# Optimization experiments

Hardware: AMD Instinct MI355X
Metric: run time of the kernel (lower is better)

## Reference

```python
import jax, jax.numpy as jnp
import numpy as np

BLOCK, HALO, HEADS = 8, 3, 4


def setup_inputs() -> dict:
    key = jax.random.key(0)
    k1, k2, k3, k4 = jax.random.split(key, 4)
    ch, d = 128, 128 // HEADS
    win = BLOCK + 2 * HALO
    return {
        "x": jax.random.normal(k1, (8, ch, 128, 128), dtype=jnp.float32),
        "qkv_w": jax.random.normal(k2, (3 * ch, ch), dtype=jnp.float32) * (2.0 / ch) ** 0.5,
        "rel_h": jax.random.normal(k3, (1, win, 1, d // 2), dtype=jnp.float32),
        "rel_w": jax.random.normal(k4, (1, 1, win, d // 2), dtype=jnp.float32),
    }


def _halo_windows(t, block, halo):
    b, c, h, w = t.shape
    win = block + 2 * halo
    nh, nw = h // block, w // block
    tp = jnp.pad(t, ((0, 0), (0, 0), (halo, halo), (halo, halo)))
    idx_h = (jnp.arange(nh) * block)[:, None] + jnp.arange(win)[None, :]
    idx_w = (jnp.arange(nw) * block)[:, None] + jnp.arange(win)[None, :]
    return tp[:, :, idx_h[:, None, :, None], idx_w[None, :, None, :]]


def reference(x, qkv_w, rel_h, rel_w):
    block, halo, heads = BLOCK, HALO, HEADS
    b, c, h, w = x.shape
    d = c // heads
    win = block + 2 * halo
    nh, nw = h // block, w // block

    # 1x1 conv (bias=False)
    qkv = jnp.einsum('bchw,oc->bohw', x, qkv_w)
    q, k, v = jnp.split(qkv, 3, axis=1)

    # q: non-overlapping blocks -> (b, nh, nw, heads, block*block, d), scaled
    q = q.reshape(b, heads, d, nh, block, nw, block)
    q = q.transpose(0, 3, 5, 1, 4, 6, 2).reshape(b, nh, nw, heads, block * block, d)
    q = q * d ** -0.5

    kw = _halo_windows(k, block, halo)
    vw = _halo_windows(v, block, halo)
    kw = kw.reshape(b, heads, d, nh, nw, win, win).transpose(0, 3, 4, 1, 5, 6, 2)
    vw = vw.reshape(b, heads, d, nh, nw, win, win).transpose(0, 3, 4, 1, 5, 6, 2)
    vw = vw.reshape(b, nh, nw, heads, win * win, d)

    # relative position bias added to keys (first half varies over rows, second over cols)
    k_h, k_w2 = jnp.split(kw, 2, axis=-1)
    kw = jnp.concatenate([k_h + rel_h, k_w2 + rel_w], axis=-1)
    kw = kw.reshape(b, nh, nw, heads, win * win, d)

    sim = jnp.einsum('...id,...jd->...ij', q, kw)
    attn = jax.nn.softmax(sim, axis=-1)
    out = jnp.einsum('...ij,...jd->...id', attn, vw)  # (b,nh,nw,heads, blk^2, d)

    # reassemble: channel = (head, d) head-major; rows = (nh, k1); cols = (nw, k2)
    out = out.reshape(b, nh, nw, heads, block, block, d)
    out = out.transpose(0, 3, 6, 1, 4, 2, 5).reshape(b, c, h, w)
    return out
```

## Files before the change

### kernel.cpp

```cpp
#include <hip/hip_runtime.h>
#include <hip/hip_bf16.h>


typedef __attribute__((ext_vector_type(8))) short bf16x8;
typedef __attribute__((ext_vector_type(4))) short bf16x4;
typedef __attribute__((ext_vector_type(4))) float f32x4;
union BF8 { bf16x8 v; unsigned u[4]; };
union BF4 { bf16x4 v; unsigned u[2]; };

#define DEVI static __device__ __forceinline__

DEVI short f2bf(float f) {
    __bf16 h = (__bf16)f;
    union { __bf16 h; short s; } c; c.h = h; return c.s;
}
DEVI unsigned pk2(float a, float b) {
    return (unsigned)(unsigned short)f2bf(a) | ((unsigned)(unsigned short)f2bf(b) << 16);
}

#if defined(__has_builtin)
#  if __has_builtin(__builtin_amdgcn_exp2f)
#    define EXP2(x) __builtin_amdgcn_exp2f(x)
#  else
#    define EXP2(x) exp2f(x)
#  endif
#else
#  define EXP2(x) exp2f(x)
#endif

#if defined(__has_builtin)
#  if __has_builtin(__builtin_amdgcn_mfma_f32_16x16x16bf16_1k)
#    define HAVE_MFMA16_1K 1
#  endif
#endif

DEVI f32x4 mfma16(bf16x4 a, bf16x4 b, f32x4 c) {
#ifdef HAVE_MFMA16_1K
    return __builtin_amdgcn_mfma_f32_16x16x16bf16_1k(a, b, c, 0, 0, 0);
#else
    f32x4 d;
    asm("v_mfma_f32_16x16x16_bf16 %0, %1, %2, %3" : "=v"(d) : "v"(a), "v"(b), "v"(c));
    return d;
#endif
}

#define QSCALE (0.17677669529663687f * 1.4426950408889634f)

__global__ void wcvt(const float* __restrict__ w, short* __restrict__ ws_w) {
    int e = blockIdx.x * 256 + threadIdx.x;
    if (e < 384 * 128) {
        float v = w[e];
        if (e < 128 * 128) v *= QSCALE;
        ws_w[e] = f2bf(v);
    }
}

__launch_bounds__(256)
__global__ void qkv_gemm(const float* __restrict__ x, const short* __restrict__ ws_w,
                         short* __restrict__ ws_q, short* __restrict__ ws_k,
                         short* __restrict__ ws_v) {
    const int blk = blockIdx.x;
    const int b = blk >> 6;
    const int pixbase = (blk & 63) << 8;
    const int tid = threadIdx.x, wv = tid >> 6, ln = tid & 63;
    const int lr = ln & 15, lg = ln >> 4;
    const int n0 = pixbase + wv * 64;
    const f32x4 zz = {0.f, 0.f, 0.f, 0.f};

    BF8 Bx[4][4];
    #pragma unroll
    for (int nt = 0; nt < 4; ++nt) {
        const int pix = n0 + nt * 16 + lr;
        #pragma unroll
        for (int ks = 0; ks < 4; ++ks) {
            const float* xp = x + (((size_t)((b << 7) + ks * 32 + lg * 8)) << 14) + pix;
            float f[8];
            #pragma unroll
            for (int e = 0; e < 8; ++e) f[e] = xp[(size_t)e << 14];
            Bx[nt][ks].u[0] = pk2(f[0], f[1]); Bx[nt][ks].u[1] = pk2(f[2], f[3]);
            Bx[nt][ks].u[2] = pk2(f[4], f[5]); Bx[nt][ks].u[3] = pk2(f[6], f[7]);
        }
    }

    for (int ot = 0; ot < 24; ++ot) {
        bf16x8 Aw[4];
        #pragma unroll
        for (int ks = 0; ks < 4; ++ks)
            Aw[ks] = *(const bf16x8*)&ws_w[(ot * 16 + lr) * 128 + ks * 32 + lg * 8];
        f32x4 acc[4];
        #pragma unroll
        for (int nt = 0; nt < 4; ++nt) {
            acc[nt] = zz;
            #pragma unroll
            for (int ks = 0; ks < 4; ++ks)
                acc[nt] = __builtin_amdgcn_mfma_f32_16x16x32_bf16(Aw[ks], Bx[nt][ks].v, acc[nt], 0, 0, 0);
        }
        if (ot < 8) {
            const int head = ot >> 1, dd0 = ((ot & 1) << 4) + lg * 4;
            #pragma unroll
            for (int nt = 0; nt < 4; ++nt) {
                const int pix = n0 + nt * 16 + lr;
                const int gr = pix >> 7, gc = pix & 127;
                const int ii = gr >> 3, jj = gc >> 3;
                const int qrow = ((gr & 7) << 3) | (gc & 7);
                size_t off = ((size_t)((((b * 16 + ii) * 16 + jj) << 2) + head) << 11) + qrow * 32 + dd0;
                *(uint2*)&ws_q[off] = make_uint2(pk2(acc[nt][0], acc[nt][1]), pk2(acc[nt][2], acc[nt][3]));
            }
        } else if (ot < 16) {
            const int head = (ot - 8) >> 1, dd0 = (((ot - 8) & 1) << 4) + lg * 4;
            const size_t kb = ((size_t)(b * 4 + head)) << 19;
            #pragma unroll
            for (int nt = 0; nt < 4; ++nt) {
                const int pix = n0 + nt * 16 + lr;
                *(uint2*)&ws_k[kb + pix * 32 + dd0] =
                    make_uint2(pk2(acc[nt][0], acc[nt][1]), pk2(acc[nt][2], acc[nt][3]));
            }
        } else {
            const int vch = ((ot - 16) << 4) + lg * 4;
            const int head = vch >> 5, dd = vch & 31;
            #pragma unroll
            for (int nt = 0; nt < 4; ++nt) {
                const int pix = n0 + nt * 16 + lr;
                const int gr = pix >> 7, gc = pix & 127;
                const size_t base = ((((size_t)(b * 4 + head) << 7) + gr) * 32 + dd) * 136 + 3 + gc;
                #pragma unroll
                for (int r = 0; r < 4; ++r) ws_v[base + r * 136] = f2bf(acc[nt][r]);
            }
        }
    }
}

template<bool EDGE>
DEVI void attn_body(int b, int i, int j, int head, int ln, int mt0,
                    const short* __restrict__ ws_q, const short* __restrict__ ws_k,
                    const short* __restrict__ ws_v,
                    const float* __restrict__ rel_h, const float* __restrict__ rel_w,
                    float* __restrict__ out) {
    const int lr = ln & 15, lg = ln >> 4;
    const f32x4 zz = {0.f, 0.f, 0.f, 0.f};
    const int bh = b * 4 + head;

    const short* qbase = ws_q + ((size_t)((((b * 16 + i) * 16 + j) << 2) + head) << 11);
    const short* kbase = ws_k + (((size_t)bh) << 19);
    const short* vbase = ws_v + (size_t)bh * (128 * 32 * 136);

    bf16x8 Bq[2];
    #pragma unroll
    for (int m = 0; m < 2; ++m)
        Bq[m] = *(const bf16x8*)&qbase[((mt0 + m) * 16 + lr) * 32 + lg * 8];

    BF8 Ah, Awf;
    #pragma unroll
    for (int wd = 0; wd < 4; ++wd) { Ah.u[wd] = 0u; Awf.u[wd] = 0u; }
    if (lr < 14) {
        if (lg < 2) {
            const float* rp = rel_h + lr * 16 + lg * 8;
            #pragma unroll
            for (int wd = 0; wd < 4; ++wd) Ah.u[wd] = pk2(rp[2 * wd], rp[2 * wd + 1]);
        } else {
            const float* rp = rel_w + lr * 16 + (lg - 2) * 8;
            #pragma unroll
            for (int wd = 0; wd < 4; ++wd) Awf.u[wd] = pk2(rp[2 * wd], rp[2 * wd + 1]);
        }
    }
    f32x4 qh4[2], qw4[2];
    #pragma unroll
    for (int m = 0; m < 2; ++m) {
        qh4[m] = __builtin_amdgcn_mfma_f32_16x16x32_bf16(Ah.v, Bq[m], zz, 0, 0, 0);
        qw4[m] = __builtin_amdgcn_mfma_f32_16x16x32_bf16(Awf.v, Bq[m], zz, 0, 0, 0);
    }
    if (lg == 3) {
        #pragma unroll
        for (int m = 0; m < 2; ++m) { qw4[m][2] = -16384.f; qw4[m][3] = -16384.f; }
    }

    BF4 Bones; Bones.u[0] = 0x3F803F80u; Bones.u[1] = 0x3F803F80u;

    const int gc   = j * 8 - 3 + lr;
    const int gcc  = EDGE ? min(max(gc, 0), 127) : gc;
    const bool gcBad = EDGE && (gc != gcc);
    const int colb = j * 8 + lg * 4;
    unsigned mmc0 = 0xFFFFFFFFu, mmc1 = 0xFFFFFFFFu;
    if (EDGE) {
        const int gc0 = colb - 3;
        const int lo = max(0, -gc0), hi = min(3, 127 - gc0);
        const unsigned bits = (lo <= hi) ? (((0xFu >> (3 - (hi - lo))) << lo) & 0xFu) : 0u;
        mmc0 = ((bits & 1u) ? 0x0000FFFFu : 0u) | ((bits & 2u) ? 0xFFFF0000u : 0u);
        mmc1 = ((bits & 4u) ? 0x0000FFFFu : 0u) | ((bits & 8u) ? 0xFFFF0000u : 0u);
    }

    f32x4 a0A[2] = {zz, zz}, a1A[2] = {zz, zz}, sAA[2] = {zz, zz};
    f32x4 a0B[2] = {zz, zz}, a1B[2] = {zz, zz}, sAB[2] = {zz, zz};

#define STEP(T, A0, A1, SA) { \
        const int gr_ = i * 8 - 3 + (T); \
        const bool grOK_ = !EDGE || ((unsigned)gr_ < 128u); \
        const int grc_ = EDGE ? min(max(gr_, 0), 127) : gr_; \
        BF8 Ak_; \
        Ak_.v = *(const bf16x8*)&kbase[((grc_ << 7) + gcc) * 32 + lg * 8]; \
        if (EDGE && (gcBad || !grOK_)) { Ak_.u[0] = 0; Ak_.u[1] = 0; Ak_.u[2] = 0; Ak_.u[3] = 0; } \
        BF4 Bv0_, Bv1_; \
        *(uint2*)Bv0_.u = *(const uint2*)&vbase[((grc_ << 5) + lr) * 136 + colb]; \
        *(uint2*)Bv1_.u = *(const uint2*)&vbase[((grc_ << 5) + 16 + lr) * 136 + colb]; \
        if (EDGE) { \
            const unsigned mm0_ = grOK_ ? mmc0 : 0u; \
            const unsigned mm1_ = grOK_ ? mmc1 : 0u; \
            Bv0_.u[0] &= mm0_; Bv0_.u[1] &= mm1_; Bv1_.u[0] &= mm0_; Bv1_.u[1] &= mm1_; \
        } \
        _Pragma("unroll") \
        for (int m = 0; m < 2; ++m) { \
            const float qh_ = __shfl(qh4[m][(T) & 3], (((T) >> 2) << 4) | lr, 64); \
            f32x4 cin_; \
            _Pragma("unroll") \
            for (int r = 0; r < 4; ++r) cin_[r] = qw4[m][r] + qh_; \
            const f32x4 p_ = __builtin_amdgcn_mfma_f32_16x16x32_bf16(Ak_.v, Bq[m], cin_, 0, 0, 0); \
            BF4 Ap_; \
            Ap_.u[0] = pk2(EXP2(p_[0]), EXP2(p_[1])); \
            Ap_.u[1] = pk2(EXP2(p_[2]), EXP2(p_[3])); \
            A0[m] = mfma16(Ap_.v, Bv0_.v, A0[m]); \
            A1[m] = mfma16(Ap_.v, Bv1_.v, A1[m]); \
            SA[m] = mfma16(Ap_.v, Bones.v, SA[m]); \
        } \
    }

    #pragma unroll
    for (int t = 0; t < 7; ++t) {
        STEP(t,     a0A, a1A, sAA)
        STEP(t + 7, a0B, a1B, sAB)
    }
#undef STEP

    #pragma unroll
    for (int m = 0; m < 2; ++m) {
        f32x4 acc0, acc1;
        #pragma unroll
        for (int r = 0; r < 4; ++r) {
            const float rinv = __builtin_amdgcn_rcpf(sAA[m][r] + sAB[m][r]);
            acc0[r] = (a0A[m][r] + a0B[m][r]) * rinv;
            acc1[r] = (a1A[m][r] + a1B[m][r]) * rinv;
        }
        const int qb = (mt0 + m) * 16 + lg * 4;
        float* op = out + (((size_t)(b * 128 + head * 32)) << 14)
                        + ((i * 8 + (qb >> 3)) << 7) + j * 8 + (qb & 7);
        *(f32x4*)(op + ((size_t)lr << 14)) = acc0;
        *(f32x4*)(op + ((size_t)(16 + lr) << 14)) = acc1;
    }
}

__launch_bounds__(256, 2)
__global__ void attn4(const short* __restrict__ ws_q, const short* __restrict__ ws_k,
                      const short* __restrict__ ws_v,
                      const float* __restrict__ rel_h, const float* __restrict__ rel_w,
                      float* __restrict__ out) {
    const int bid = blockIdx.x;
    const int x = bid & 7, n = bid >> 3;
    const int g = x + ((n >> 7) << 3);
    const int l = n & 127;
    const int b = g >> 2;
    const int i = ((g & 3) << 2) | (l >> 5);
    const int j = (l >> 1) & 15;
    const int half = l & 1;
    const int head = threadIdx.x >> 6, ln = threadIdx.x & 63;
    if (i == 0 || i == 15 || j == 0 || j == 15)
        attn_body<true>(b, i, j, head, ln, half * 2, ws_q, ws_k, ws_v, rel_h, rel_w, out);
    else
        attn_body<false>(b, i, j, head, ln, half * 2, ws_q, ws_k, ws_v, rel_h, rel_w, out);
}

__launch_bounds__(256, 2)
__global__ void halo_attn(const float* __restrict__ x,
                          const float* __restrict__ qkv_w,
                          const float* __restrict__ relh_g,
                          const float* __restrict__ relw_g,
                          float* __restrict__ out)
{
    const int blk  = blockIdx.x;
    const int head = blk & 3;
    const int j    = (blk >> 2) & 15;
    const int i    = (blk >> 6) & 15;
    const int b    = blk >> 10;
    const int tid = threadIdx.x;
    const int wv  = tid >> 6;
    const int ln  = tid & 63;
    const int lr  = ln & 15;
    const int lg  = ln >> 4;

    __shared__ __align__(16) union { short xs[112*128]; short pbuf[64*224]; } XP;
    __shared__ __align__(16) short kbuf[208*32];
    __shared__ __align__(16) short vbufT[32*224];
    __shared__ __align__(16) short qbuf[64*32];
    __shared__ float smax[4*64];
    __shared__ float ssum[4*64];
    __shared__ float relh[224];
    __shared__ float relw[224];

    for (int t = tid; t < 32*224/2; t += 256) ((int*)vbufT)[t] = 0;
    for (int t = tid; t < 224; t += 256) { relh[t] = relh_g[t]; relw[t] = relw_g[t]; }

    bf16x8 Bw[6][4];
    #pragma unroll
    for (int n = 0; n < 6; ++n) {
        const int obase = (n < 2) ? head*32 + n*16
                        : (n < 4) ? 128 + head*32 + (n-2)*16
                                  : 256 + head*32 + (n-4)*16;
        const float* wp0 = qkv_w + (obase + lr)*128;
        #pragma unroll
        for (int ks = 0; ks < 4; ++ks) {
            const float* wp = wp0 + ks*32 + lg*8;
            bf16x8 f;
            #pragma unroll
            for (int e = 0; e < 8; ++e) f[e] = f2bf(wp[e]);
            Bw[n][ks] = f;
        }
    }

    for (int ph = 0; ph < 2; ++ph) {
        __syncthreads();
        for (int t = tid; t < 112*128; t += 256) {
            const int ch = t / 112;
            const int p  = t - ch*112;
            float val = 0.f;
            if (p < 98) {
                const int P  = ph*98 + p;
                const int wr = P / 14, wc = P - wr*14;
                const int gr = i*8 - 3 + wr, gc = j*8 - 3 + wc;
                if ((unsigned)gr < 128u && (unsigned)gc < 128u)
                    val = x[((b*128 + ch)*128 + gr)*128 + gc];
            }
            XP.xs[p*128 + (ch & 7) + 8*((ch >> 3) ^ (p & 15))] = f2bf(val);
        }
        __syncthreads();

        for (int mt = wv; mt < 7; mt += 4) {
            const int row = mt*16 + lr;
            bf16x8 A[4];
            #pragma unroll
            for (int ks = 0; ks < 4; ++ks)
                A[ks] = *(const bf16x8*)&XP.xs[row*128 + 8*((ks*4 + lg) ^ (row & 15))];
            #pragma unroll
            for (int n = 0; n < 6; ++n) {
                f32x4 acc = {0.f, 0.f, 0.f, 0.f};
                #pragma unroll
                for (int ks = 0; ks < 4; ++ks)
                    acc = __builtin_amdgcn_mfma_f32_16x16x32_bf16(A[ks], Bw[n][ks], acc, 0, 0, 0);
                #pragma unroll
                for (int r = 0; r < 4; ++r) {
                    const int p = mt*16 + lg*4 + r;
                    if (p >= 98) continue;
                    const int P  = ph*98 + p;
                    const int wr = P / 14, wc = P - wr*14;
                    const float val = acc[r];
                    if (n < 2) {
                        if (wr >= 3 && wr <= 10 && wc >= 3 && wc <= 10) {
                            const int qi = (wr-3)*8 + (wc-3);
                            const int dd = n*16 + lr;
                            qbuf[qi*32 + (dd & 7) + 8*((dd >> 3) ^ ((qi >> 1) & 3))] =
                                f2bf(val * 0.17677669529663687f);
                        }
                    } else if (n < 4) {
                        const int dd = (n-2)*16 + lr;
                        const float bias = (dd < 16) ? relh[wr*16 + dd] : relw[wc*16 + dd - 16];
                        kbuf[P*32 + (dd & 7) + 8*((dd >> 3) ^ ((P >> 1) & 3))] = f2bf(val + bias);
                    } else {
                        const int dd = (n-4)*16 + lr;
                        vbufT[dd*224 + (P & 7) + 8*((P >> 3) ^ ((dd >> 1) & 3))] = f2bf(val);
                    }
                }
            }
        }
    }
    __syncthreads();

    bf16x8 Aq[4];
    #pragma unroll
    for (int mt = 0; mt < 4; ++mt) {
        const int row = mt*16 + lr;
        Aq[mt] = *(const bf16x8*)&qbuf[row*32 + 8*(lg ^ ((row >> 1) & 3))];
    }

    f32x4 sim[4][4];
    #pragma unroll
    for (int ntl = 0; ntl < 4; ++ntl) {
        const int nt = wv + ntl*4;
        if (nt > 12) continue;
        const int P = nt*16 + lr;
        const bf16x8 Bk = *(const bf16x8*)&kbuf[P*32 + 8*(lg ^ ((P >> 1) & 3))];
        #pragma unroll
        for (int mt = 0; mt < 4; ++mt) {
            const f32x4 z = {0.f, 0.f, 0.f, 0.f};
            sim[ntl][mt] = __builtin_amdgcn_mfma_f32_16x16x32_bf16(Aq[mt], Bk, z, 0, 0, 0);
        }
    }

    for (int t = tid; t < 64*224/2; t += 256) ((int*)XP.pbuf)[t] = 0;

    #pragma unroll
    for (int mt = 0; mt < 4; ++mt)
    #pragma unroll
    for (int r = 0; r < 4; ++r) {
        float m = -1e30f;
        #pragma unroll
        for (int ntl = 0; ntl < 4; ++ntl) {
            const int nt = wv + ntl*4;
            if (nt > 12) continue;
            const int key = nt*16 + lr;
            if (key < 196) m = fmaxf(m, sim[ntl][mt][r]);
        }
        #pragma unroll
        for (int off = 1; off < 16; off <<= 1)
            m = fmaxf(m, __shfl_xor(m, off, 64));
        if (lr == 0) smax[wv*64 + mt*16 + lg*4 + r] = m;
    }
    __syncthreads();

    #pragma unroll
    for (int mt = 0; mt < 4; ++mt)
    #pragma unroll
    for (int r = 0; r < 4; ++r) {
        const int qrow = mt*16 + lg*4 + r;
        const float gm = fmaxf(fmaxf(smax[qrow], smax[64+qrow]),
                               fmaxf(smax[128+qrow], smax[192+qrow]));
        float s = 0.f;
        #pragma unroll
        for (int ntl = 0; ntl < 4; ++ntl) {
            const int nt = wv + ntl*4;
            if (nt > 12) continue;
            const int key = nt*16 + lr;
            float e = (key < 196) ? __expf(sim[ntl][mt][r] - gm) : 0.f;
            sim[ntl][mt][r] = e;
            s += e;
        }
        #pragma unroll
        for (int off = 1; off < 16; off <<= 1)
            s += __shfl_xor(s, off, 64);
        if (lr == 0) ssum[wv*64 + qrow] = s;
    }
    __syncthreads();

    #pragma unroll
    for (int mt = 0; mt < 4; ++mt)
    #pragma unroll
    for (int r = 0; r < 4; ++r) {
        const int qrow = mt*16 + lg*4 + r;
        const float rinv = 1.f / (ssum[qrow] + ssum[64+qrow] + ssum[128+qrow] + ssum[192+qrow]);
        #pragma unroll
        for (int ntl = 0; ntl < 4; ++ntl) {
            const int nt = wv + ntl*4;
            if (nt > 12) continue;
            const int key = nt*16 + lr;
            XP.pbuf[qrow*224 + (key & 7) + 8*((key >> 3) ^ ((qrow >> 1) & 3))] =
                f2bf(sim[ntl][mt][r] * rinv);
        }
    }
    __syncthreads();

    f32x4 oacc[2] = {{0.f,0.f,0.f,0.f},{0.f,0.f,0.f,0.f}};
    const int mt = wv;
    #pragma unroll
    for (int ks = 0; ks < 7; ++ks) {
        const int row = mt*16 + lr;
        const int g = ks*4 + lg;
        const bf16x8 Ap = *(const bf16x8*)&XP.pbuf[row*224 + 8*(g ^ ((row >> 1) & 3))];
        #pragma unroll
        for (int n = 0; n < 2; ++n) {
            const int dd = n*16 + lr;
            const bf16x8 Bv = *(const bf16x8*)&vbufT[dd*224 + 8*(g ^ ((dd >> 1) & 3))];
            oacc[n] = __builtin_amdgcn_mfma_f32_16x16x32_bf16(Ap, Bv, oacc[n], 0, 0, 0);
        }
    }

    #pragma unroll
    for (int n = 0; n < 2; ++n) {
        const int dd = n*16 + lr;
        const int c  = head*32 + dd;
        const int qb = mt*16 + lg*4;
        const int rb = qb >> 3, cb = qb & 7;
        float* op = out + ((b*128 + c)*128 + (i*8 + rb))*128 + j*8 + cb;
        *(f32x4*)op = oacc[n];
    }
}

extern "C" void kernel_launch(void* const* d_in, const int* in_sizes, int n_in,
                              void* d_out, int out_size, void* d_ws, size_t ws_size,
                              hipStream_t stream)
{
    const float* x  = (const float*)d_in[0];
    const float* w  = (const float*)d_in[1];
    const float* rh = (const float*)d_in[2];
    const float* rw = (const float*)d_in[3];
    float* o = (float*)d_out;

    const size_t Q_ELEMS = (size_t)8192 * 2048;
    const size_t K_ELEMS = (size_t)32 * 16384 * 32;
    const size_t V_ELEMS = (size_t)32 * 128 * 32 * 136;
    const size_t W_ELEMS = (size_t)384 * 128;
    const size_t NEED = (Q_ELEMS + K_ELEMS + V_ELEMS + W_ELEMS) * 2 + 1024;

    if (ws_size >= NEED) {
        short* ws_q = (short*)d_ws;
        short* ws_k = ws_q + Q_ELEMS;
        short* ws_v = ws_k + K_ELEMS;
        short* ws_w = ws_v + V_ELEMS;
        wcvt<<<dim3(192), dim3(256), 0, stream>>>(w, ws_w);
        qkv_gemm<<<dim3(512), dim3(256), 0, stream>>>(x, ws_w, ws_q, ws_k, ws_v);
        attn4<<<dim3(4096), dim3(256), 0, stream>>>(ws_q, ws_k, ws_v, rh, rw, o);
    } else {
        halo_attn<<<dim3(8192), dim3(256), 0, stream>>>(x, w, rh, rw, o);
    }
}
```

Measured before the change: 113.4 us.

## Store V in quad-column tiled layout via transposed MFMA for vector stores

```diff
diff --git a/kernel.cpp b/kernel.cpp
--- a/kernel.cpp
+++ b/kernel.cpp
@@ -87,44 +87,55 @@
         #pragma unroll
         for (int ks = 0; ks < 4; ++ks)
             Aw[ks] = *(const bf16x8*)&ws_w[(ot * 16 + lr) * 128 + ks * 32 + lg * 8];
-        f32x4 acc[4];
-        #pragma unroll
-        for (int nt = 0; nt < 4; ++nt) {
-            acc[nt] = zz;
-            #pragma unroll
-            for (int ks = 0; ks < 4; ++ks)
-                acc[nt] = __builtin_amdgcn_mfma_f32_16x16x32_bf16(Aw[ks], Bx[nt][ks].v, acc[nt], 0, 0, 0);
-        }
-        if (ot < 8) {
-            const int head = ot >> 1, dd0 = ((ot & 1) << 4) + lg * 4;
+
+        if (ot < 16) {
+            f32x4 acc[4];
             #pragma unroll
             for (int nt = 0; nt < 4; ++nt) {
-                const int pix = n0 + nt * 16 + lr;
-                const int gr = pix >> 7, gc = pix & 127;
-                const int ii = gr >> 3, jj = gc >> 3;
-                const int qrow = ((gr & 7) << 3) | (gc & 7);
-                size_t off = ((size_t)((((b * 16 + ii) * 16 + jj) << 2) + head) << 11) + qrow * 32 + dd0;
-                *(uint2*)&ws_q[off] = make_uint2(pk2(acc[nt][0], acc[nt][1]), pk2(acc[nt][2], acc[nt][3]));
+                acc[nt] = zz;
+                #pragma unroll
+                for (int ks = 0; ks < 4; ++ks)
+                    acc[nt] = __builtin_amdgcn_mfma_f32_16x16x32_bf16(Aw[ks], Bx[nt][ks].v, acc[nt], 0, 0, 0);
             }
-        } else if (ot < 16) {
-            const int head = (ot - 8) >> 1, dd0 = (((ot - 8) & 1) << 4) + lg * 4;
-            const size_t kb = ((size_t)(b * 4 + head)) << 19;
-            #pragma unroll
-            for (int nt = 0; nt < 4; ++nt) {
-                const int pix = n0 + nt * 16 + lr;
-                *(uint2*)&ws_k[kb + pix * 32 + dd0] =
-                    make_uint2(pk2(acc[nt][0], acc[nt][1]), pk2(acc[nt][2], acc[nt][3]));
+            if (ot < 8) {
+                const int head = ot >> 1, dd0 = ((ot & 1) << 4) + lg * 4;
+                #pragma unroll
+                for (int nt = 0; nt < 4; ++nt) {
+                    const int pix = n0 + nt * 16 + lr;
+                    const int gr = pix >> 7, gc = pix & 127;
+                    const int ii = gr >> 3, jj = gc >> 3;
+                    const int qrow = ((gr & 7) << 3) | (gc & 7);
+                    size_t off = ((size_t)((((b * 16 + ii) * 16 + jj) << 2) + head) << 11) + qrow * 32 + dd0;
+                    *(uint2*)&ws_q[off] = make_uint2(pk2(acc[nt][0], acc[nt][1]), pk2(acc[nt][2], acc[nt][3]));
+                }
+            } else {
+                const int head = (ot - 8) >> 1, dd0 = (((ot - 8) & 1) << 4) + lg * 4;
+                const size_t kb = ((size_t)(b * 4 + head)) << 19;
+                #pragma unroll
+                for (int nt = 0; nt < 4; ++nt) {
+                    const int pix = n0 + nt * 16 + lr;
+                    *(uint2*)&ws_k[kb + pix * 32 + dd0] =
+                        make_uint2(pk2(acc[nt][0], acc[nt][1]), pk2(acc[nt][2], acc[nt][3]));
+                }
             }
         } else {
-            const int vch = ((ot - 16) << 4) + lg * 4;
-            const int head = vch >> 5, dd = vch & 31;
+            const int vch = ((ot - 16) << 4) + lr;
+            const int headv = vch >> 5, dv = vch & 31;
+            f32x4 accT[4];
             #pragma unroll
             for (int nt = 0; nt < 4; ++nt) {
-                const int pix = n0 + nt * 16 + lr;
-                const int gr = pix >> 7, gc = pix & 127;
-                const size_t base = ((((size_t)(b * 4 + head) << 7) + gr) * 32 + dd) * 136 + 3 + gc;
+                accT[nt] = zz;
                 #pragma unroll
-                for (int r = 0; r < 4; ++r) ws_v[base + r * 136] = f2bf(acc[nt][r]);
+                for (int ks = 0; ks < 4; ++ks)
+                    accT[nt] = __builtin_amdgcn_mfma_f32_16x16x32_bf16(Bx[nt][ks].v, Aw[ks], accT[nt], 0, 0, 0);
+            }
+            #pragma unroll
+            for (int nt = 0; nt < 4; ++nt) {
+                const int pixq = n0 + nt * 16 + lg * 4;
+                const int gr = pixq >> 7, gcq = (pixq & 127) >> 2;
+                const size_t idx = ((((size_t)(b * 4 + headv) * 128 + gr) * 32 + gcq) * 32 + dv) * 4;
+                *(uint2*)&ws_v[idx] =
+                    make_uint2(pk2(accT[nt][0], accT[nt][1]), pk2(accT[nt][2], accT[nt][3]));
             }
         }
     }
@@ -142,7 +153,7 @@
 
     const short* qbase = ws_q + ((size_t)((((b * 16 + i) * 16 + j) << 2) + head) << 11);
     const short* kbase = ws_k + (((size_t)bh) << 19);
-    const short* vbase = ws_v + (size_t)bh * (128 * 32 * 136);
+    const short* vbase = ws_v + (((size_t)bh) << 19);
 
     bf16x8 Bq[2];
     #pragma unroll
@@ -179,10 +190,16 @@
     const int gc   = j * 8 - 3 + lr;
     const int gcc  = EDGE ? min(max(gc, 0), 127) : gc;
     const bool gcBad = EDGE && (gc != gcc);
-    const int colb = j * 8 + lg * 4;
+    const int qAraw = 2 * j + lg - 1;
+    const int qA = EDGE ? min(max(qAraw, 0), 31) : qAraw;
+    const int qB = EDGE ? min(qAraw + 1, 31) : (qAraw + 1);
+    const int oA0 = (qA * 32 + lr) * 4;
+    const int oA1 = oA0 + 64;
+    const int oB0 = (qB * 32 + lr) * 4;
+    const int oB1 = oB0 + 64;
     unsigned mmc0 = 0xFFFFFFFFu, mmc1 = 0xFFFFFFFFu;
     if (EDGE) {
-        const int gc0 = colb - 3;
+        const int gc0 = j * 8 - 3 + lg * 4;
         const int lo = max(0, -gc0), hi = min(3, 127 - gc0);
         const unsigned bits = (lo <= hi) ? (((0xFu >> (3 - (hi - lo))) << lo) & 0xFu) : 0u;
         mmc0 = ((bits & 1u) ? 0x0000FFFFu : 0u) | ((bits & 2u) ? 0xFFFF0000u : 0u);
@@ -199,9 +216,16 @@
         BF8 Ak_; \
         Ak_.v = *(const bf16x8*)&kbase[((grc_ << 7) + gcc) * 32 + lg * 8]; \
         if (EDGE && (gcBad || !grOK_)) { Ak_.u[0] = 0; Ak_.u[1] = 0; Ak_.u[2] = 0; Ak_.u[3] = 0; } \
+        const int vrow_ = grc_ << 12; \
+        const uint2 aA0_ = *(const uint2*)&vbase[vrow_ + oA0]; \
+        const uint2 aA1_ = *(const uint2*)&vbase[vrow_ + oA1]; \
+        const unsigned bB0_ = *(const unsigned short*)&vbase[vrow_ + oB0]; \
+        const unsigned bB1_ = *(const unsigned short*)&vbase[vrow_ + oB1]; \
         BF4 Bv0_, Bv1_; \
-        *(uint2*)Bv0_.u = *(const uint2*)&vbase[((grc_ << 5) + lr) * 136 + colb]; \
-        *(uint2*)Bv1_.u = *(const uint2*)&vbase[((grc_ << 5) + 16 + lr) * 136 + colb]; \
+        Bv0_.u[0] = __builtin_amdgcn_alignbit(aA0_.y, aA0_.x, 16); \
+        Bv0_.u[1] = __builtin_amdgcn_alignbit(bB0_, aA0_.y, 16); \
+        Bv1_.u[0] = __builtin_amdgcn_alignbit(aA1_.y, aA1_.x, 16); \
+        Bv1_.u[1] = __builtin_amdgcn_alignbit(bB1_, aA1_.y, 16); \
         if (EDGE) { \
             const unsigned mm0_ = grOK_ ? mmc0 : 0u; \
             const unsigned mm1_ = grOK_ ? mmc1 : 0u; \
@@ -492,7 +516,7 @@
 
     const size_t Q_ELEMS = (size_t)8192 * 2048;
     const size_t K_ELEMS = (size_t)32 * 16384 * 32;
-    const size_t V_ELEMS = (size_t)32 * 128 * 32 * 136;
+    const size_t V_ELEMS = (size_t)32 * 128 * 32 * 32 * 4;
     const size_t W_ELEMS = (size_t)384 * 128;
     const size_t NEED = (Q_ELEMS + K_ELEMS + V_ELEMS + W_ELEMS) * 2 + 1024;
 
```

Measured after the change: 104.7 us (median of 3 runs). 1.08x faster.
